# Performance work log

Hardware: AMD Instinct MI355X
Metric: run time of the kernel (lower is better)

The kernel has to match this reference:

```python
import jax, jax.numpy as jnp
import numpy as np

N = 1024
H = 128
W = 128
TANX = 0.5
TANY = 0.5
FX = W / (2.0 * TANX)
FY = H / (2.0 * TANY)
SCALE_MOD = 1.0

# spherical-harmonic constants (match 3DGS CUDA)
C0 = 0.28209479177387814
C1 = 0.4886025119029199
C2 = (1.0925484305920792, -1.0925484305920792, 0.31539156525252005, -1.0925484305920792, 0.5462742152960396)
C3 = (-0.5900435899266435, 2.890611442640554, -0.4570457994644658, 0.3731763325901154, -0.4570457994644658, 1.445305721320277, -0.5900435899266435)


def _quat_to_rot(q):
    q = q / jnp.linalg.norm(q, axis=-1, keepdims=True)
    r, x, y, z = q[:, 0], q[:, 1], q[:, 2], q[:, 3]
    row0 = jnp.stack([1 - 2 * (y * y + z * z), 2 * (x * y - r * z), 2 * (x * z + r * y)], -1)
    row1 = jnp.stack([2 * (x * y + r * z), 1 - 2 * (x * x + z * z), 2 * (y * z - r * x)], -1)
    row2 = jnp.stack([2 * (x * z - r * y), 2 * (y * z + r * x), 1 - 2 * (x * x + y * y)], -1)
    return jnp.stack([row0, row1, row2], 1)  # [n,3,3]


def _sh_to_rgb(sh, d):
    x, y, z = d[:, 0:1], d[:, 1:2], d[:, 2:3]
    res = C0 * sh[:, 0]
    res = res - C1 * y * sh[:, 1] + C1 * z * sh[:, 2] - C1 * x * sh[:, 3]
    xx, yy, zz = x * x, y * y, z * z
    xy, yz, xz = x * y, y * z, x * z
    res = (res + C2[0] * xy * sh[:, 4] + C2[1] * yz * sh[:, 5]
           + C2[2] * (2 * zz - xx - yy) * sh[:, 6] + C2[3] * xz * sh[:, 7]
           + C2[4] * (xx - yy) * sh[:, 8])
    res = (res + C3[0] * y * (3 * xx - yy) * sh[:, 9] + C3[1] * xy * z * sh[:, 10]
           + C3[2] * y * (4 * zz - xx - yy) * sh[:, 11]
           + C3[3] * z * (2 * zz - 3 * xx - 3 * yy) * sh[:, 12]
           + C3[4] * x * (4 * zz - xx - yy) * sh[:, 13]
           + C3[5] * z * (xx - yy) * sh[:, 14] + C3[6] * x * (xx - 3 * yy) * sh[:, 15])
    return jnp.maximum(res + 0.5, 0.0)


def _rasterize(means3D, opacities, shs, scales, rotations, viewmatrix, projmatrix, campos, bg):
    n = means3D.shape[0]
    dt = means3D.dtype
    hom = jnp.concatenate([means3D, jnp.ones((n, 1), dt)], -1)
    p_view = hom @ viewmatrix                      # row-vector convention
    depth = p_view[:, 2]
    valid = depth > 0.2
    p_hom = hom @ projmatrix
    p_proj = p_hom[:, :3] / (p_hom[:, 3:4] + 1e-7)
    # 3D covariance: Sigma = R diag(s^2) R^T
    R = _quat_to_rot(rotations)
    M = R * (scales * SCALE_MOD)[:, None, :]
    Sigma = jnp.einsum('nij,nkj->nik', M, M)
    # EWA projection to 2D covariance
    tz = jnp.where(valid, depth, 1.0)
    txtz = jnp.clip(p_view[:, 0] / tz, -1.3 * TANX, 1.3 * TANX) * tz
    tytz = jnp.clip(p_view[:, 1] / tz, -1.3 * TANY, 1.3 * TANY) * tz
    zero = jnp.zeros_like(tz)
    J = jnp.stack([
        jnp.stack([FX / tz, zero, -FX * txtz / (tz * tz)], -1),
        jnp.stack([zero, FY / tz, -FY * tytz / (tz * tz)], -1)], 1)  # [n,2,3]
    Wr = viewmatrix[:3, :3].T
    T2 = jnp.einsum('nij,jk->nik', J, Wr)
    cov2 = jnp.einsum('nij,njk,nlk->nil', T2, Sigma, T2)
    a = cov2[:, 0, 0] + 0.3
    b = cov2[:, 0, 1]
    c = cov2[:, 1, 1] + 0.3
    det = a * c - b * b
    valid = valid & (det > 0)
    inv_det = 1.0 / jnp.where(det > 0, det, 1.0)
    conA, conB, conC = c * inv_det, -b * inv_det, a * inv_det
    mid = 0.5 * (a + c)
    lam1 = mid + jnp.sqrt(jnp.maximum(0.1, mid * mid - det))
    radii = jnp.where(valid, jnp.ceil(3.0 * jnp.sqrt(lam1)), 0.0).astype(jnp.int32)
    # NDC -> pixel centers (ndc2Pix)
    xy = ((p_proj[:, :2] + 1.0) * jnp.array([W, H], dt) - 1.0) * 0.5
    # SH evaluation -> RGB
    dirs = means3D - campos[None, :]
    dirs = dirs / jnp.linalg.norm(dirs, axis=-1, keepdims=True)
    colors = _sh_to_rgb(shs, dirs)                 # [n,3]
    # global front-to-back depth sort
    order = jnp.argsort(jnp.where(valid, depth, jnp.inf))
    conA, conB, conC = conA[order], conB[order], conC[order]
    xyo = xy[order]
    opo = opacities[order, 0]
    colo = colors[order]
    vo = valid[order]
    # dense per-pixel evaluation (tile binning is a perf optimization only)
    yy, xx = jnp.meshgrid(jnp.arange(H, dtype=dt), jnp.arange(W, dtype=dt), indexing='ij')
    pxf = xx.reshape(-1)
    pyf = yy.reshape(-1)
    dx = xyo[:, 0:1] - pxf[None, :]                # [n, HW]
    dy = xyo[:, 1:2] - pyf[None, :]
    power = -0.5 * (conA[:, None] * dx * dx + conC[:, None] * dy * dy) - conB[:, None] * dx * dy
    alpha = jnp.minimum(0.99, opo[:, None] * jnp.exp(jnp.minimum(power, 0.0)))
    alpha = jnp.where((power <= 0) & (alpha >= 1.0 / 255.0) & vo[:, None], alpha, 0.0)
    Tinc = jnp.cumprod(1.0 - alpha, axis=0)        # T after gaussian i
    Texc = jnp.concatenate([jnp.ones((1, H * W), dt), Tinc[:-1]], 0)  # T before gaussian i
    ae = jnp.where(Tinc >= 1e-4, alpha, 0.0)       # early-termination threshold as in CUDA
    weight = Texc * ae
    img = jnp.einsum('np,nc->cp', weight, colo)
    Tfin = jnp.prod(1.0 - ae, axis=0)
    img = img + bg[:, None] * Tfin[None, :]
    return img.reshape(3, H, W), radii


def setup_inputs() -> dict:
    key = jax.random.key(0)
    ks = jax.random.split(key, 6)
    means3D = jax.random.uniform(ks[0], (N, 3)) * jnp.array([4.0, 4.0, 4.0]) + jnp.array([-2.0, -2.0, 2.0])
    means2D = jnp.zeros((N, 3), jnp.float32)
    opacities = jax.random.uniform(ks[1], (N, 1)) * 0.8 + 0.2
    shs = jax.random.normal(ks[2], (N, 16, 3)) * 0.3
    scales = jax.random.uniform(ks[3], (N, 3)) * 0.1 + 0.02
    rotations = jax.random.normal(ks[4], (N, 4))
    viewmatrix = jnp.eye(4, dtype=jnp.float32)     # camera at origin looking +z
    znear, zfar = 0.01, 100.0
    projmatrix = jnp.array([[1.0 / TANX, 0, 0, 0],
                            [0, 1.0 / TANY, 0, 0],
                            [0, 0, zfar / (zfar - znear), 1.0],
                            [0, 0, -zfar * znear / (zfar - znear), 0]], jnp.float32)
    campos = jnp.zeros(3, jnp.float32)
    bg = jnp.zeros(3, jnp.float32)
    return {"means3D": means3D, "means2D": means2D, "opacities": opacities, "shs": shs,
            "scales": scales, "rotations": rotations, "viewmatrix": viewmatrix,
            "projmatrix": projmatrix, "campos": campos, "bg": bg}


def reference(means3D, means2D, opacities, shs, scales, rotations, viewmatrix, projmatrix, campos, bg):
    color, radii = _rasterize(means3D, opacities, shs, scales, rotations, viewmatrix, projmatrix, campos, bg)
    return color, radii
```

## Files before the change

kernel.cpp:

```cpp
#include <hip/hip_runtime.h>
#include <stdint.h>

#define N_G   1024
#define H_IMG 128
#define W_IMG 128
#define TILE  8
#define TILES_X (W_IMG / TILE)
#define N_TILES (TILES_X * (H_IMG/TILE))
#define FXc   128.0f
#define FYc   128.0f

__global__ __launch_bounds__(64) void gauss_tile_kernel(
    const float* __restrict__ means3D, const float* __restrict__ opac,
    const float* __restrict__ shs,     const float* __restrict__ scales,
    const float* __restrict__ rot,     const float* __restrict__ vm,
    const float* __restrict__ pm,      const float* __restrict__ campos,
    const float* __restrict__ bg,
    float* __restrict__ out)
{
    __shared__ float gxA[N_G], gyA[N_G], cAA[N_G], cBA[N_G], cCA[N_G], opA[N_G];
    __shared__ unsigned long long keys[N_G];
    __shared__ float colR[64], colG[64], colB[64];

    const int lane = threadIdx.x;
    const int bid  = blockIdx.x;
    const int tx = bid & (TILES_X - 1), ty = bid / TILES_X;
    const float x0 = (float)(tx * TILE), x1 = x0 + (float)(TILE - 1);
    const float y0 = (float)(ty * TILE), y1 = y0 + (float)(TILE - 1);
    const float px = x0 + (float)(lane & (TILE - 1));
    const float py = y0 + (float)(lane / TILE);

    float rgx[16], rgy[16], rrc[16];
    unsigned int rdp[16];

    for (int k = 0; k < N_G / 64; ++k) {
        const int n = k * 64 + lane;

        float mx = means3D[n*3+0], my = means3D[n*3+1], mz = means3D[n*3+2];

        float pv0   = mx*vm[0] + my*vm[4] + mz*vm[8]  + vm[12];
        float pv1   = mx*vm[1] + my*vm[5] + mz*vm[9]  + vm[13];
        float depth = mx*vm[2] + my*vm[6] + mz*vm[10] + vm[14];
        bool dvalid = depth > 0.2f;

        float ph0 = mx*pm[0] + my*pm[4] + mz*pm[8]  + pm[12];
        float ph1 = mx*pm[1] + my*pm[5] + mz*pm[9]  + pm[13];
        float ph3 = mx*pm[3] + my*pm[7] + mz*pm[11] + pm[15];
        float invw = 1.0f / (ph3 + 1e-7f);
        float pp0 = ph0 * invw, pp1 = ph1 * invw;

        float4 q = *(const float4*)(rot + n*4);
        float qn = sqrtf(q.x*q.x + q.y*q.y + q.z*q.z + q.w*q.w);
        float qr = q.x/qn, qx = q.y/qn, qy = q.z/qn, qz = q.w/qn;
        float R00 = 1.f - 2.f*(qy*qy + qz*qz), R01 = 2.f*(qx*qy - qr*qz), R02 = 2.f*(qx*qz + qr*qy);
        float R10 = 2.f*(qx*qy + qr*qz), R11 = 1.f - 2.f*(qx*qx + qz*qz), R12 = 2.f*(qy*qz - qr*qx);
        float R20 = 2.f*(qx*qz - qr*qy), R21 = 2.f*(qy*qz + qr*qx), R22 = 1.f - 2.f*(qx*qx + qy*qy);

        float s0 = scales[n*3+0], s1 = scales[n*3+1], s2 = scales[n*3+2];
        float M00=R00*s0, M01=R01*s1, M02=R02*s2;
        float M10=R10*s0, M11=R11*s1, M12=R12*s2;
        float M20=R20*s0, M21=R21*s1, M22=R22*s2;

        float S00 = M00*M00 + M01*M01 + M02*M02;
        float S01 = M00*M10 + M01*M11 + M02*M12;
        float S02 = M00*M20 + M01*M21 + M02*M22;
        float S11 = M10*M10 + M11*M11 + M12*M12;
        float S12 = M10*M20 + M11*M21 + M12*M22;
        float S22 = M20*M20 + M21*M21 + M22*M22;

        float tz   = dvalid ? depth : 1.0f;
        float txtz = fminf(fmaxf(pv0 / tz, -0.65f), 0.65f) * tz;
        float tytz = fminf(fmaxf(pv1 / tz, -0.65f), 0.65f) * tz;
        float J00 = FXc / tz, J02 = -FXc * txtz / (tz*tz);
        float J11 = FYc / tz, J12 = -FYc * tytz / (tz*tz);

        float T20k0 = J00*vm[0] + J02*vm[2];
        float T20k1 = J00*vm[4] + J02*vm[6];
        float T20k2 = J00*vm[8] + J02*vm[10];
        float T21k0 = J11*vm[1] + J12*vm[2];
        float T21k1 = J11*vm[5] + J12*vm[6];
        float T21k2 = J11*vm[9] + J12*vm[10];

        float U00 = T20k0*S00 + T20k1*S01 + T20k2*S02;
        float U01 = T20k0*S01 + T20k1*S11 + T20k2*S12;
        float U02 = T20k0*S02 + T20k1*S12 + T20k2*S22;
        float U10 = T21k0*S00 + T21k1*S01 + T21k2*S02;
        float U11 = T21k0*S01 + T21k1*S11 + T21k2*S12;
        float U12 = T21k0*S02 + T21k1*S12 + T21k2*S22;
        float cov00 = U00*T20k0 + U01*T20k1 + U02*T20k2;
        float cov01 = U00*T21k0 + U01*T21k1 + U02*T21k2;
        float cov11 = U10*T21k0 + U11*T21k1 + U12*T21k2;

        float a = cov00 + 0.3f, b = cov01, c = cov11 + 0.3f;
        float det = a*c - b*b;
        bool valid = dvalid && (det > 0.0f);
        float inv_det = (det > 0.0f) ? (1.0f / det) : 1.0f;
        float conA = c * inv_det, conB = -b * inv_det, conC = a * inv_det;

        float mid  = 0.5f * (a + c);
        float lam1 = mid + sqrtf(fmaxf(0.1f, mid*mid - det));
        if (bid == 0)
            out[3*H_IMG*W_IMG + n] = valid ? ceilf(3.0f * sqrtf(lam1)) : 0.0f;

        float gx = ((pp0 + 1.0f) * (float)W_IMG - 1.0f) * 0.5f;
        float gy = ((pp1 + 1.0f) * (float)H_IMG - 1.0f) * 0.5f;

        float op = opac[n];
        float op255 = op * 255.0f;
        float rc2 = (valid && op255 > 1.0f) ? (2.0f * logf(op255) * lam1 * 1.01f + 1.0f)
                                            : -1.0f;

        gxA[n] = gx; gyA[n] = gy; cAA[n] = conA; cBA[n] = conB;
        cCA[n] = conC; opA[n] = op;
        rgx[k] = gx; rgy[k] = gy; rrc[k] = rc2;
        rdp[k] = __float_as_uint(depth);
    }
    __syncthreads();

    int cnt = 0;
    for (int k = 0; k < N_G / 64; ++k) {
        float cx = fminf(fmaxf(rgx[k], x0), x1) - rgx[k];
        float cy = fminf(fmaxf(rgy[k], y0), y1) - rgy[k];
        bool pass = (cx*cx + cy*cy) <= rrc[k];
        unsigned long long mask = __ballot(pass);
        if (pass) {
            int pos = cnt + __popcll(mask & ((1ull << lane) - 1ull));
            keys[pos] = ((unsigned long long)rdp[k] << 32) | (unsigned int)(k*64 + lane);
        }
        cnt += (int)__popcll(mask);
    }
    const int M = cnt;
    __syncthreads();

    int P = 1; while (P < M) P <<= 1;
    for (int i = M + lane; i < P; i += 64) keys[i] = ~0ull;
    __syncthreads();
    for (int k = 2; k <= P; k <<= 1) {
        for (int j = k >> 1; j > 0; j >>= 1) {
            for (int i = lane; i < P; i += 64) {
                int l = i ^ j;
                if (l > i) {
                    unsigned long long ka = keys[i], kb = keys[l];
                    bool asc = ((i & k) == 0);
                    if ((ka > kb) == asc) { keys[i] = kb; keys[l] = ka; }
                }
            }
            __syncthreads();
        }
    }

    const float cpx = campos[0], cpy = campos[1], cpz = campos[2];
    float T = 1.0f, Tfin = 1.0f, cr = 0.f, cg = 0.f, cb = 0.f;
    bool live = true;

    for (int base = 0; base < M; base += 64) {
        int j2 = base + lane;
        if (j2 < M) {
            int idx = (int)(keys[j2] & 0xFFFFFFFFu);
            float mx = means3D[idx*3+0], my = means3D[idx*3+1], mz = means3D[idx*3+2];
            float dxm = mx - cpx, dym = my - cpy, dzm = mz - cpz;
            float dn = sqrtf(dxm*dxm + dym*dym + dzm*dzm);
            float sx = dxm/dn, sy = dym/dn, sz = dzm/dn;
            float xx = sx*sx, yy = sy*sy, zz = sz*sz;
            float xy = sx*sy, yz = sy*sz, xz = sx*sz;
            const float4* sh4 = (const float4*)(shs + idx*48);
            float shf[48];
            #pragma unroll
            for (int t = 0; t < 12; ++t) {
                float4 v = sh4[t];
                shf[t*4+0]=v.x; shf[t*4+1]=v.y; shf[t*4+2]=v.z; shf[t*4+3]=v.w;
            }
            float col[3];
            #pragma unroll
            for (int ch = 0; ch < 3; ++ch) {
                float res = 0.28209479177387814f * shf[0*3+ch]
                    - 0.4886025119029199f * sy * shf[1*3+ch]
                    + 0.4886025119029199f * sz * shf[2*3+ch]
                    - 0.4886025119029199f * sx * shf[3*3+ch]
                    + 1.0925484305920792f  * xy * shf[4*3+ch]
                    + (-1.0925484305920792f) * yz * shf[5*3+ch]
                    + 0.31539156525252005f * (2.f*zz - xx - yy) * shf[6*3+ch]
                    + (-1.0925484305920792f) * xz * shf[7*3+ch]
                    + 0.5462742152960396f  * (xx - yy) * shf[8*3+ch]
                    + (-0.5900435899266435f) * sy * (3.f*xx - yy) * shf[9*3+ch]
                    + 2.890611442640554f   * xy * sz * shf[10*3+ch]
                    + (-0.4570457994644658f) * sy * (4.f*zz - xx - yy) * shf[11*3+ch]
                    + 0.3731763325901154f  * sz * (2.f*zz - 3.f*xx - 3.f*yy) * shf[12*3+ch]
                    + (-0.4570457994644658f) * sx * (4.f*zz - xx - yy) * shf[13*3+ch]
                    + 1.445305721320277f   * sz * (xx - yy) * shf[14*3+ch]
                    + (-0.5900435899266435f) * sx * (xx - 3.f*yy) * shf[15*3+ch];
                col[ch] = fmaxf(res + 0.5f, 0.0f);
            }
            colR[lane] = col[0]; colG[lane] = col[1]; colB[lane] = col[2];
        }
        __syncthreads();

        int nb = min(64, M - base);
        for (int j = 0; j < nb; ++j) {
            int idx = (int)(keys[base + j] & 0xFFFFFFFFu);
            float gx = gxA[idx], gy = gyA[idx];
            float A  = cAA[idx], B  = cBA[idx], C = cCA[idx], op = opA[idx];
            float dx = gx - px, dy = gy - py;
            float power = -0.5f * (A*dx*dx + C*dy*dy) - B*dx*dy;
            float alpha = fminf(0.99f, op * __expf(power));
            if (live && power <= 0.0f && alpha >= (1.0f/255.0f)) {
                float Tnew = T * (1.0f - alpha);
                if (Tnew < 1e-4f) {
                    live = false;
                } else {
                    float w = T * alpha;
                    cr += w * colR[j]; cg += w * colG[j]; cb += w * colB[j];
                    Tfin *= (1.0f - alpha);
                    T = Tnew;
                }
            }
        }
        __syncthreads();
        if (__ballot(live) == 0ull) break;
    }

    int p = (int)py * W_IMG + (int)px;
    out[p]                 = cr + bg[0] * Tfin;
    out[H_IMG*W_IMG + p]   = cg + bg[1] * Tfin;
    out[2*H_IMG*W_IMG + p] = cb + bg[2] * Tfin;
}

extern "C" void kernel_launch(void* const* d_in, const int* in_sizes, int n_in,
                              void* d_out, int out_size, void* d_ws, size_t ws_size,
                              hipStream_t stream) {
    const float* means3D = (const float*)d_in[0];
    const float* opac    = (const float*)d_in[2];
    const float* shs     = (const float*)d_in[3];
    const float* scales  = (const float*)d_in[4];
    const float* rot     = (const float*)d_in[5];
    const float* vm      = (const float*)d_in[6];
    const float* pm      = (const float*)d_in[7];
    const float* campos  = (const float*)d_in[8];
    const float* bg      = (const float*)d_in[9];

    gauss_tile_kernel<<<N_TILES, 64, 0, stream>>>(
        means3D, opac, shs, scales, rot, vm, pm, campos, bg, (float*)d_out);
}
```

Before: 105.3 us.

## Widen blocks to 256 threads for preprocessing, culling, sort and SH colour

```diff
diff --git a/kernel.cpp b/kernel.cpp
--- a/kernel.cpp
+++ b/kernel.cpp
@@ -7,10 +7,11 @@
 #define TILE  8
 #define TILES_X (W_IMG / TILE)
 #define N_TILES (TILES_X * (H_IMG/TILE))
+#define NT    256
 #define FXc   128.0f
 #define FYc   128.0f
 
-__global__ __launch_bounds__(64) void gauss_tile_kernel(
+__global__ __launch_bounds__(NT) void gauss_tile_kernel(
     const float* __restrict__ means3D, const float* __restrict__ opac,
     const float* __restrict__ shs,     const float* __restrict__ scales,
     const float* __restrict__ rot,     const float* __restrict__ vm,
@@ -18,23 +19,23 @@
     const float* __restrict__ bg,
     float* __restrict__ out)
 {
-    __shared__ float gxA[N_G], gyA[N_G], cAA[N_G], cBA[N_G], cCA[N_G], opA[N_G];
+    __shared__ float gxA[N_G], gyA[N_G], cAA[N_G], cBA[N_G], cCA[N_G],
+                     opA[N_G], rcA[N_G];
+    __shared__ unsigned int dpA[N_G];
     __shared__ unsigned long long keys[N_G];
-    __shared__ float colR[64], colG[64], colB[64];
-
-    const int lane = threadIdx.x;
-    const int bid  = blockIdx.x;
+    __shared__ float colR[N_G], colG[N_G], colB[N_G];
+    __shared__ int cnt;
+
+    const int t   = threadIdx.x;
+    const int bid = blockIdx.x;
     const int tx = bid & (TILES_X - 1), ty = bid / TILES_X;
     const float x0 = (float)(tx * TILE), x1 = x0 + (float)(TILE - 1);
     const float y0 = (float)(ty * TILE), y1 = y0 + (float)(TILE - 1);
-    const float px = x0 + (float)(lane & (TILE - 1));
-    const float py = y0 + (float)(lane / TILE);
-
-    float rgx[16], rgy[16], rrc[16];
-    unsigned int rdp[16];
-
-    for (int k = 0; k < N_G / 64; ++k) {
-        const int n = k * 64 + lane;
+
+    if (t == 0) cnt = 0;
+
+    for (int k = 0; k < N_G / NT; ++k) {
+        const int n = k * NT + t;
 
         float mx = means3D[n*3+0], my = means3D[n*3+1], mz = means3D[n*3+2];
 
@@ -95,49 +96,47 @@
         float det = a*c - b*b;
         bool valid = dvalid && (det > 0.0f);
         float inv_det = (det > 0.0f) ? (1.0f / det) : 1.0f;
-        float conA = c * inv_det, conB = -b * inv_det, conC = a * inv_det;
 
         float mid  = 0.5f * (a + c);
         float lam1 = mid + sqrtf(fmaxf(0.1f, mid*mid - det));
         if (bid == 0)
             out[3*H_IMG*W_IMG + n] = valid ? ceilf(3.0f * sqrtf(lam1)) : 0.0f;
 
-        float gx = ((pp0 + 1.0f) * (float)W_IMG - 1.0f) * 0.5f;
-        float gy = ((pp1 + 1.0f) * (float)H_IMG - 1.0f) * 0.5f;
-
         float op = opac[n];
         float op255 = op * 255.0f;
         float rc2 = (valid && op255 > 1.0f) ? (2.0f * logf(op255) * lam1 * 1.01f + 1.0f)
                                             : -1.0f;
 
-        gxA[n] = gx; gyA[n] = gy; cAA[n] = conA; cBA[n] = conB;
-        cCA[n] = conC; opA[n] = op;
-        rgx[k] = gx; rgy[k] = gy; rrc[k] = rc2;
-        rdp[k] = __float_as_uint(depth);
-    }
-    __syncthreads();
-
-    int cnt = 0;
-    for (int k = 0; k < N_G / 64; ++k) {
-        float cx = fminf(fmaxf(rgx[k], x0), x1) - rgx[k];
-        float cy = fminf(fmaxf(rgy[k], y0), y1) - rgy[k];
-        bool pass = (cx*cx + cy*cy) <= rrc[k];
-        unsigned long long mask = __ballot(pass);
-        if (pass) {
-            int pos = cnt + __popcll(mask & ((1ull << lane) - 1ull));
-            keys[pos] = ((unsigned long long)rdp[k] << 32) | (unsigned int)(k*64 + lane);
-        }
-        cnt += (int)__popcll(mask);
-    }
+        gxA[n] = ((pp0 + 1.0f) * (float)W_IMG - 1.0f) * 0.5f;
+        gyA[n] = ((pp1 + 1.0f) * (float)H_IMG - 1.0f) * 0.5f;
+        cAA[n] = c * inv_det;
+        cBA[n] = -b * inv_det;
+        cCA[n] = a * inv_det;
+        opA[n] = op;
+        rcA[n] = rc2;
+        dpA[n] = __float_as_uint(depth);
+    }
+    __syncthreads();
+
+    for (int k = 0; k < N_G / NT; ++k) {
+        const int n = k * NT + t;
+        float gx = gxA[n], gy = gyA[n];
+        float cx = fminf(fmaxf(gx, x0), x1) - gx;
+        float cy = fminf(fmaxf(gy, y0), y1) - gy;
+        if (cx*cx + cy*cy <= rcA[n]) {
+            int slot = atomicAdd(&cnt, 1);
+            keys[slot] = ((unsigned long long)dpA[n] << 32) | (unsigned int)n;
+        }
+    }
+    __syncthreads();
     const int M = cnt;
-    __syncthreads();
 
     int P = 1; while (P < M) P <<= 1;
-    for (int i = M + lane; i < P; i += 64) keys[i] = ~0ull;
+    for (int i = M + t; i < P; i += NT) keys[i] = ~0ull;
     __syncthreads();
     for (int k = 2; k <= P; k <<= 1) {
         for (int j = k >> 1; j > 0; j >>= 1) {
-            for (int i = lane; i < P; i += 64) {
+            for (int i = t; i < P; i += NT) {
                 int l = i ^ j;
                 if (l > i) {
                     unsigned long long ka = keys[i], kb = keys[l];
@@ -150,54 +149,58 @@
     }
 
     const float cpx = campos[0], cpy = campos[1], cpz = campos[2];
-    float T = 1.0f, Tfin = 1.0f, cr = 0.f, cg = 0.f, cb = 0.f;
-    bool live = true;
-
-    for (int base = 0; base < M; base += 64) {
-        int j2 = base + lane;
-        if (j2 < M) {
-            int idx = (int)(keys[j2] & 0xFFFFFFFFu);
-            float mx = means3D[idx*3+0], my = means3D[idx*3+1], mz = means3D[idx*3+2];
-            float dxm = mx - cpx, dym = my - cpy, dzm = mz - cpz;
-            float dn = sqrtf(dxm*dxm + dym*dym + dzm*dzm);
-            float sx = dxm/dn, sy = dym/dn, sz = dzm/dn;
-            float xx = sx*sx, yy = sy*sy, zz = sz*sz;
-            float xy = sx*sy, yz = sy*sz, xz = sx*sz;
-            const float4* sh4 = (const float4*)(shs + idx*48);
-            float shf[48];
-            #pragma unroll
-            for (int t = 0; t < 12; ++t) {
-                float4 v = sh4[t];
-                shf[t*4+0]=v.x; shf[t*4+1]=v.y; shf[t*4+2]=v.z; shf[t*4+3]=v.w;
-            }
-            float col[3];
-            #pragma unroll
-            for (int ch = 0; ch < 3; ++ch) {
-                float res = 0.28209479177387814f * shf[0*3+ch]
-                    - 0.4886025119029199f * sy * shf[1*3+ch]
-                    + 0.4886025119029199f * sz * shf[2*3+ch]
-                    - 0.4886025119029199f * sx * shf[3*3+ch]
-                    + 1.0925484305920792f  * xy * shf[4*3+ch]
-                    + (-1.0925484305920792f) * yz * shf[5*3+ch]
-                    + 0.31539156525252005f * (2.f*zz - xx - yy) * shf[6*3+ch]
-                    + (-1.0925484305920792f) * xz * shf[7*3+ch]
-                    + 0.5462742152960396f  * (xx - yy) * shf[8*3+ch]
-                    + (-0.5900435899266435f) * sy * (3.f*xx - yy) * shf[9*3+ch]
-                    + 2.890611442640554f   * xy * sz * shf[10*3+ch]
-                    + (-0.4570457994644658f) * sy * (4.f*zz - xx - yy) * shf[11*3+ch]
-                    + 0.3731763325901154f  * sz * (2.f*zz - 3.f*xx - 3.f*yy) * shf[12*3+ch]
-                    + (-0.4570457994644658f) * sx * (4.f*zz - xx - yy) * shf[13*3+ch]
-                    + 1.445305721320277f   * sz * (xx - yy) * shf[14*3+ch]
-                    + (-0.5900435899266435f) * sx * (xx - 3.f*yy) * shf[15*3+ch];
-                col[ch] = fmaxf(res + 0.5f, 0.0f);
-            }
-            colR[lane] = col[0]; colG[lane] = col[1]; colB[lane] = col[2];
-        }
-        __syncthreads();
-
-        int nb = min(64, M - base);
-        for (int j = 0; j < nb; ++j) {
-            int idx = (int)(keys[base + j] & 0xFFFFFFFFu);
+    for (int s = t; s < M; s += NT) {
+        int idx = (int)(keys[s] & 0xFFFFFFFFu);
+        float mx = means3D[idx*3+0], my = means3D[idx*3+1], mz = means3D[idx*3+2];
+        float dxm = mx - cpx, dym = my - cpy, dzm = mz - cpz;
+        float dn = sqrtf(dxm*dxm + dym*dym + dzm*dzm);
+        float sx = dxm/dn, sy = dym/dn, sz = dzm/dn;
+        float xx = sx*sx, yy = sy*sy, zz = sz*sz;
+        float xy = sx*sy, yz = sy*sz, xz = sx*sz;
+
+        float bb[16];
+        bb[0]  = 0.28209479177387814f;
+        bb[1]  = -0.4886025119029199f * sy;
+        bb[2]  =  0.4886025119029199f * sz;
+        bb[3]  = -0.4886025119029199f * sx;
+        bb[4]  =  1.0925484305920792f * xy;
+        bb[5]  = -1.0925484305920792f * yz;
+        bb[6]  =  0.31539156525252005f * (2.f*zz - xx - yy);
+        bb[7]  = -1.0925484305920792f * xz;
+        bb[8]  =  0.5462742152960396f * (xx - yy);
+        bb[9]  = -0.5900435899266435f * sy * (3.f*xx - yy);
+        bb[10] =  2.890611442640554f  * xy * sz;
+        bb[11] = -0.4570457994644658f * sy * (4.f*zz - xx - yy);
+        bb[12] =  0.3731763325901154f * sz * (2.f*zz - 3.f*xx - 3.f*yy);
+        bb[13] = -0.4570457994644658f * sx * (4.f*zz - xx - yy);
+        bb[14] =  1.445305721320277f  * sz * (xx - yy);
+        bb[15] = -0.5900435899266435f * sx * (xx - 3.f*yy);
+
+        float acc[3] = {0.f, 0.f, 0.f};
+        const float4* sh4 = (const float4*)(shs + idx*48);
+        #pragma unroll
+        for (int u = 0; u < 12; ++u) {
+            float4 v = sh4[u];
+            int f = 4*u;
+            acc[(f+0)%3] += bb[(f+0)/3] * v.x;
+            acc[(f+1)%3] += bb[(f+1)/3] * v.y;
+            acc[(f+2)%3] += bb[(f+2)/3] * v.z;
+            acc[(f+3)%3] += bb[(f+3)/3] * v.w;
+        }
+        colR[s] = fmaxf(acc[0] + 0.5f, 0.f);
+        colG[s] = fmaxf(acc[1] + 0.5f, 0.f);
+        colB[s] = fmaxf(acc[2] + 0.5f, 0.f);
+    }
+    __syncthreads();
+
+    if (t < 64) {
+        const float px = x0 + (float)(t & (TILE - 1));
+        const float py = y0 + (float)(t / TILE);
+        float T = 1.0f, Tfin = 1.0f, cr = 0.f, cg = 0.f, cb = 0.f;
+        bool live = true;
+
+        for (int j = 0; j < M; ++j) {
+            int idx = (int)(keys[j] & 0xFFFFFFFFu);
             float gx = gxA[idx], gy = gyA[idx];
             float A  = cAA[idx], B  = cBA[idx], C = cCA[idx], op = opA[idx];
             float dx = gx - px, dy = gy - py;
@@ -214,15 +217,14 @@
                     T = Tnew;
                 }
             }
-        }
-        __syncthreads();
-        if (__ballot(live) == 0ull) break;
-    }
-
-    int p = (int)py * W_IMG + (int)px;
-    out[p]                 = cr + bg[0] * Tfin;
-    out[H_IMG*W_IMG + p]   = cg + bg[1] * Tfin;
-    out[2*H_IMG*W_IMG + p] = cb + bg[2] * Tfin;
+            if (__ballot(live) == 0ull) break;
+        }
+
+        int p = (int)py * W_IMG + (int)px;
+        out[p]                 = cr + bg[0] * Tfin;
+        out[H_IMG*W_IMG + p]   = cg + bg[1] * Tfin;
+        out[2*H_IMG*W_IMG + p] = cb + bg[2] * Tfin;
+    }
 }
 
 extern "C" void kernel_launch(void* const* d_in, const int* in_sizes, int n_in,
@@ -238,6 +240,6 @@
     const float* campos  = (const float*)d_in[8];
     const float* bg      = (const float*)d_in[9];
 
-    gauss_tile_kernel<<<N_TILES, 64, 0, stream>>>(
+    gauss_tile_kernel<<<N_TILES, NT, 0, stream>>>(
         means3D, opac, shs, scales, rot, vm, pm, campos, bg, (float*)d_out);
 }
```

After: 89.72 us. 14.8% less time.
